# Optimization experiments

Hardware: AMD Instinct MI355X
Metric: run time of the kernel (lower is better)

Reference implementation:

```python
import jax, jax.numpy as jnp
import numpy as np
jax.config.update("jax_enable_x64", True)

B, S, E, H, L, FF = 2, 1024, 768, 12, 4, 2048
MAX_THOUGHT_LEN = 3
LN_EPS = 1e-5

def _sinusoidal_pe(max_len, d):
    pos = np.arange(max_len)[:, None]
    div = np.exp(np.arange(0, d, 2) * (-np.log(10000.0) / d))
    pe = np.zeros((max_len, d), np.float32)
    pe[:, 0::2] = np.sin(pos * div)
    pe[:, 1::2] = np.cos(pos * div)
    return jnp.asarray(pe)

def _build_mask(Smax, thoughts_taken, n_tokens):
    # Vectorized equivalent of the torch loop building the block-causal mask.
    bs = thoughts_taken + 1
    i = np.arange(Smax)[:, None]
    j = np.arange(Smax)[None, :]
    same_block = (i // bs == j // bs) & (i // bs < n_tokens) & ((i % bs) >= (j % bs))
    start_vis = ((j % bs) == 0) & (j // bs < n_tokens) & (i > j) & (i < n_tokens * bs)
    allowed = same_block | start_vis
    # TransformerEncoder canonicalizes the bool mask: True (disallowed) -> -inf additive
    return jnp.asarray(np.where(allowed, 0.0, -np.inf).astype(np.float64))

def _layernorm(x, w, b):
    mu = jnp.mean(x, -1, keepdims=True)
    var = jnp.mean((x - mu) ** 2, -1, keepdims=True)
    return (x - mu) / jnp.sqrt(var + LN_EPS) * w + b

def setup_inputs() -> dict:
    key = jax.random.key(0)
    ks = jax.random.split(key, 8)
    f32 = jnp.float32
    return {
        "x": jax.random.normal(ks[0], (B, S, E), f32),
        "padding_mask": jnp.zeros((B, S), bool),
        "thought_pe": jax.random.normal(ks[1], (MAX_THOUGHT_LEN + 1, E), f32),
        "Wqkv": jax.random.normal(ks[2], (L, 3 * E, E), f32) * (E ** -0.5),
        "bqkv": jnp.zeros((L, 3 * E), f32),
        "W1": jax.random.normal(ks[3], (L, FF, E), f32) * (E ** -0.5),
        "b1": jnp.zeros((L, FF), f32),
        "W2": jax.random.normal(ks[4], (L, E, FF), f32) * (FF ** -0.5),
        "b2": jnp.zeros((L, E), f32),
        "ln1_w": jnp.ones((L, E), f32), "ln1_b": jnp.zeros((L, E), f32),
        "ln2_w": jnp.ones((L, E), f32), "ln2_b": jnp.zeros((L, E), f32),
        "lnf_w": jnp.ones((E,), f32), "lnf_b": jnp.zeros((E,), f32),
        "thoughts_taken": 1,
        "real_token_count": 512,
    }

def reference(x, padding_mask, thought_pe, Wqkv, bqkv, W1, b1, W2, b2,
              ln1_w, ln1_b, ln2_w, ln2_b, lnf_w, lnf_b,
              thoughts_taken, real_token_count):
    # NOTE: padding_mask is accepted but unused, matching the custom layer.
    nt = thoughts_taken + 1
    pe = _sinusoidal_pe(S, E)
    # DualPositionalEncoding (eval mode -> dropout is identity)
    h = x[:, : real_token_count * nt].reshape(B, real_token_count, nt, E)
    h = h + pe[:real_token_count][None, :, None, :] + thought_pe[:nt][None, None, :, :]
    h = h.reshape(B, real_token_count * nt, E)
    pad = S - real_token_count * nt
    if pad > 0:
        h = jnp.pad(h, ((0, 0), (0, pad), (0, 0)))
    mask = _build_mask(S, thoughts_taken, real_token_count)
    scale = 1.0 / jnp.sqrt(jnp.float64(E // H))
    for l in range(L):
        # manual fp64 attention, exactly as the torch layer
        s64 = h.astype(jnp.float64)
        qkv = s64 @ Wqkv[l].astype(jnp.float64).T + bqkv[l].astype(jnp.float64)
        q, k, v = jnp.split(qkv, 3, axis=-1)
        rh = lambda t: t.reshape(B, S, H, E // H).transpose(0, 2, 1, 3)
        q, k, v = rh(q), rh(k), rh(v)
        scores = jnp.einsum("bhqd,bhkd->bhqk", q, k) * scale + mask
        attn = jax.nn.softmax(scores, axis=-1)
        ao = jnp.einsum("bhqk,bhkd->bhqd", attn, v).transpose(0, 2, 1, 3).reshape(B, S, E)
        # NOTE: no out_proj -- the custom forward skips self_attn.out_proj
        h = _layernorm(h + ao.astype(h.dtype), ln1_w[l], ln1_b[l])
        ff = jax.nn.gelu(h @ W1[l].T + b1[l], approximate=False) @ W2[l].T + b2[l]
        h = _layernorm(h + ff, ln2_w[l], ln2_b[l])
        h = jnp.nan_to_num(h)
    return _layernorm(h, lnf_w, lnf_b)
```

## Files before the change

kernel.cpp:

```cpp
#include <hip/hip_runtime.h>
#include <math.h>

#define SEQ 1024
#define EMB 768
#define NHEAD 12
#define HDIM 64
#define NLAYER 4
#define FFDIM 2048
#define BATCH 2
#define ROWS (BATCH * SEQ)
#define BH (BATCH * NHEAD)
#define NCHUNK 2
#define CTILES 8

using f16 = _Float16;
using f16x4 = __attribute__((ext_vector_type(4))) _Float16;
using f16x8 = __attribute__((ext_vector_type(8))) _Float16;
using f32x4 = __attribute__((ext_vector_type(4))) float;
using f32x16 = __attribute__((ext_vector_type(16))) float;
typedef unsigned long long u64;

__device__ inline void gload16(const void* g, void* l) {
    __builtin_amdgcn_global_load_lds((const __attribute__((address_space(1))) unsigned*)g,
                                     (__attribute__((address_space(3))) unsigned*)l, 16, 0, 0);
}

__global__ void prep_kernel(const float* __restrict__ Wq, int na,
                            const float* __restrict__ W1, int nb,
                            const float* __restrict__ W2, int nc,
                            f16* __restrict__ oq, f16* __restrict__ o1, f16* __restrict__ o2,
                            const float* __restrict__ x,
                            const float* __restrict__ tpe,
                            float* __restrict__ h32,
                            f16* __restrict__ h16,
                            u64* __restrict__ mtab,
                            const int* __restrict__ tt_p,
                            const int* __restrict__ rtc_p) {
    const int ncast = na + nb + nc;
    const int nembed = BATCH * SEQ * EMB;
    const int nmask = SEQ * 16;
    const int total = ncast + nembed + nmask;
    const int nt = *tt_p + 1;
    const int rtc = *rtc_p;
    for (int i = blockIdx.x * blockDim.x + threadIdx.x; i < total;
         i += gridDim.x * blockDim.x) {
        if (i < ncast) {
            const float* src;
            f16* dst;
            int off;
            if (i < na)            { src = Wq; dst = oq; off = i; }
            else if (i < na + nb)  { src = W1; dst = o1; off = i - na; }
            else                   { src = W2; dst = o2; off = i - na - nb; }
            float4 v = ((const float4*)src)[off];
            f16x4 o;
            o[0] = (f16)v.x; o[1] = (f16)v.y; o[2] = (f16)v.z; o[3] = (f16)v.w;
            ((f16x4*)dst)[off] = o;
        } else if (i < ncast + nembed) {
            int idx = i - ncast;
            int e = idx % EMB;
            int s = (idx / EMB) % SEQ;
            float val;
            if (s < rtc * nt) {
                int p = s / nt;
                int t = s % nt;
                int i2 = e & ~1;
                float div = __expf((float)i2 * -0.0119926314f);
                float ang = (float)p * div;
                float pe = (e & 1) ? __cosf(ang) : __sinf(ang);
                val = x[idx] + pe + tpe[t * EMB + e];
            } else {
                val = 0.0f;
            }
            h32[idx] = val;
            h16[idx] = (f16)val;
        } else {
            int idx = i - ncast - nembed;
            int ii = idx >> 4, jt = idx & 15;
            int id = ii / nt, im = ii % nt;
            int iok = (ii < rtc * nt);
            u64 m = 0;
            for (int k = 0; k < 64; k++) {
                int j = jt * 64 + k;
                int jd = j / nt, jm = j % nt;
                bool same = (id == jd) && (id < rtc) && (im >= jm);
                bool sv   = (jm == 0) && (jd < rtc) && (ii > j) && iok;
                if (same || sv) m |= (1ull << k);
            }
            mtab[idx] = m;
        }
    }
}

template<int ACT, int OUT>
__global__ __launch_bounds__(512) void gemm_f16(const f16* __restrict__ A,
                                                const f16* __restrict__ W,
                                                const float* __restrict__ bias,
                                                f16* __restrict__ Ch,
                                                f16* __restrict__ vtg,
                                                int M, int N, int K) {
    __shared__ f16 As[2][128 * 64];
    __shared__ f16 Ws[2][128 * 64];
    const int tid = threadIdx.x, lane = tid & 63, wave = tid >> 6;
    const int gx = gridDim.x;
    const int nwg = gx * gridDim.y;
    int orig = blockIdx.y * gx + blockIdx.x;
    int nid = (nwg & 7) ? orig : ((orig & 7) * (nwg >> 3) + (orig >> 3));
    const int bm = (nid / gx) * 128, bn = (nid % gx) * 128;
    const int l31 = lane & 31, l32 = lane >> 5;
    const int wm = (wave >> 1) * 32, wn = (wave & 1) * 64;
    const int srow = lane >> 3, sslot = lane & 7;
    const int klen = K / gridDim.z;
    const int kbeg = blockIdx.z * klen;
    const int nsteps = klen >> 6;

    f32x16 acc[2];
#pragma unroll
    for (int ni = 0; ni < 2; ni++)
#pragma unroll
        for (int e = 0; e < 16; e++) acc[ni][e] = 0.f;

#pragma unroll
    for (int i = 0; i < 2; i++) {
        int R0 = wave * 16 + i * 8;
        int row = R0 + srow;
        int gs = (sslot ^ (row & 7)) << 3;
        gload16(A + (size_t)(bm + row) * K + kbeg + gs, As[0] + R0 * 64);
        gload16(W + (size_t)(bn + row) * K + kbeg + gs, Ws[0] + R0 * 64);
    }
    __syncthreads();

    int cur = 0;
    for (int t = 0; t < nsteps; t++) {
        if (t + 1 < nsteps) {
            int k1 = kbeg + (t + 1) * 64;
            int nxt = cur ^ 1;
#pragma unroll
            for (int i = 0; i < 2; i++) {
                int R0 = wave * 16 + i * 8;
                int row = R0 + srow;
                int gs = (sslot ^ (row & 7)) << 3;
                gload16(A + (size_t)(bm + row) * K + k1 + gs, As[nxt] + R0 * 64);
                gload16(W + (size_t)(bn + row) * K + k1 + gs, Ws[nxt] + R0 * 64);
            }
        }
#pragma unroll
        for (int ks = 0; ks < 4; ks++) {
            int kslot = ks * 2 + l32;
            f16x8 a, b[2];
            {
                int row = wm + l31;
                a = *(const f16x8*)(As[cur] + row * 64 + ((kslot ^ (row & 7)) << 3));
            }
#pragma unroll
            for (int ni = 0; ni < 2; ni++) {
                int row = wn + ni * 32 + l31;
                b[ni] = *(const f16x8*)(Ws[cur] + row * 64 + ((kslot ^ (row & 7)) << 3));
            }
#pragma unroll
            for (int ni = 0; ni < 2; ni++)
                acc[ni] = __builtin_amdgcn_mfma_f32_32x32x16_f16(a, b[ni], acc[ni], 0, 0, 0);
        }
        __syncthreads();
        cur ^= 1;
    }

#pragma unroll
    for (int ni = 0; ni < 2; ni++) {
        int nbase = bn + wn + ni * 32;
        int n = nbase + l31;
        if (OUT == 3) {
            f16* dst = Ch + (size_t)blockIdx.z * ROWS * N;
#pragma unroll
            for (int reg = 0; reg < 16; reg++) {
                int m = bm + wm + (reg & 3) + 8 * (reg >> 2) + 4 * l32;
                dst[(size_t)m * N + n] = (f16)acc[ni][reg];
            }
        } else {
            float bv = bias[n];
            if (OUT != 2 || nbase < 2 * EMB) {
                int cstride = (OUT == 2) ? 2 * EMB : N;
#pragma unroll
                for (int reg = 0; reg < 16; reg++) {
                    int m = bm + wm + (reg & 3) + 8 * (reg >> 2) + 4 * l32;
                    float v = acc[ni][reg] + bv;
                    if (ACT) v = 0.5f * v * (1.0f + erff(v * 0.70710678118654752f));
                    Ch[(size_t)m * cstride + n] = (f16)v;
                }
            } else {
                int d = n - 2 * EMB;
                int hh = d >> 6, dd = d & 63;
#pragma unroll
                for (int q = 0; q < 4; q++) {
                    int m0 = bm + wm + 8 * q + 4 * l32;
                    int bb = m0 >> 10, s0 = m0 & (SEQ - 1);
                    f16x4 pack;
#pragma unroll
                    for (int r = 0; r < 4; r++) pack[r] = (f16)(acc[ni][4 * q + r] + bv);
                    *(f16x4*)(vtg + ((size_t)((bb * NHEAD + hh) * HDIM + dd)) * SEQ + s0) = pack;
                }
            }
        }
    }
}

__global__ __launch_bounds__(256) void attn_part(const f16* __restrict__ qk,
                                                 const f16* __restrict__ vtg,
                                                 const u64* __restrict__ mtab,
                                                 f16* __restrict__ po,
                                                 float* __restrict__ pm,
                                                 float* __restrict__ pl) {
    const int c = blockIdx.x;
    const int qt = blockIdx.y;
    if (c * CTILES > qt) return;
    const int bh = blockIdx.z;
    const int b = bh / NHEAD, hh = bh % NHEAD;
    const int q0 = qt * 64;
    const int jt_beg = c * CTILES, jt_end = min(qt, c * CTILES + CTILES - 1);

    __shared__ f16 Qs[64 * 64];
    __shared__ f16 Ks[2][64 * 64];
    __shared__ f16 VT[2][64 * 64];
    __shared__ f16 Ps[4 * 16 * 64];

    const int tid = threadIdx.x, lane = tid & 63, wave = tid >> 6;
    const int l15 = lane & 15, l16 = lane >> 4;
    const int RS = 2 * EMB;
    const f16* vth = vtg + (size_t)(b * NHEAD + hh) * HDIM * SEQ;
    const float SCALE2 = 0.125f * 1.44269504088896f;

#pragma unroll
    for (int it = 0; it < 2; it++) {
        int R0 = wave * 16 + it * 8;
        int row = R0 + (lane >> 3), slot = lane & 7;
        int gs = (slot ^ (row & 7)) << 3;
        gload16(qk + (size_t)(b * SEQ + q0 + row) * RS + hh * HDIM + gs, Qs + R0 * 64);
        gload16(qk + (size_t)(b * SEQ + jt_beg * 64 + row) * RS + EMB + hh * HDIM + gs,
                Ks[0] + R0 * 64);
        gload16(vth + (size_t)row * SEQ + jt_beg * 64 + gs, VT[0] + R0 * 64);
    }
    __syncthreads();

    f16x8 qa[2];
#pragma unroll
    for (int ks = 0; ks < 2; ks++) {
        int row = wave * 16 + l15;
        int kslot = l16 + ks * 4;
        qa[ks] = *(const f16x8*)(Qs + row * 64 + ((kslot ^ (row & 7)) << 3));
    }

    f16x8 ones;
#pragma unroll
    for (int i = 0; i < 8; i++) ones[i] = (f16)1.0f;

    float mrow[4];
    f32x4 o[4], osum;
    int iglob[4];
#pragma unroll
    for (int r = 0; r < 4; r++) {
        mrow[r] = -1e30f;
        iglob[r] = q0 + wave * 16 + l16 * 4 + r;
    }
#pragma unroll
    for (int nf = 0; nf < 4; nf++) o[nf] = (f32x4){0.f, 0.f, 0.f, 0.f};
    osum = (f32x4){0.f, 0.f, 0.f, 0.f};

    for (int jt = jt_beg; jt <= jt_end; jt++) {
        const int cur = (jt - jt_beg) & 1;
        if (jt < jt_end) {
            const int nxt = cur ^ 1;
            const int jn0 = (jt + 1) * 64;
#pragma unroll
            for (int it = 0; it < 2; it++) {
                int R0 = wave * 16 + it * 8;
                int row = R0 + (lane >> 3), slot = lane & 7;
                int gs = (slot ^ (row & 7)) << 3;
                gload16(qk + (size_t)(b * SEQ + jn0 + row) * RS + EMB + hh * HDIM + gs,
                        Ks[nxt] + R0 * 64);
                gload16(vth + (size_t)row * SEQ + jn0 + gs, VT[nxt] + R0 * 64);
            }
        }

        unsigned mlo[4], mhi[4];
#pragma unroll
        for (int r = 0; r < 4; r++) {
            u64 mk = mtab[iglob[r] * 16 + jt];
            mlo[r] = (unsigned)mk;
            mhi[r] = (unsigned)(mk >> 32);
        }

        f32x4 s[4];
        __builtin_amdgcn_s_setprio(1);
#pragma unroll
        for (int nf = 0; nf < 4; nf++) {
            s[nf] = (f32x4){0.f, 0.f, 0.f, 0.f};
#pragma unroll
            for (int ks = 0; ks < 2; ks++) {
                int row = nf * 16 + l15;
                int kslot = l16 + ks * 4;
                f16x8 kb = *(const f16x8*)(Ks[cur] + row * 64 + ((kslot ^ (row & 7)) << 3));
                s[nf] = __builtin_amdgcn_mfma_f32_16x16x32_f16(qa[ks], kb, s[nf], 0, 0, 0);
            }
        }
        __builtin_amdgcn_s_setprio(0);

        float p[4][4];
        float tmax[4] = {-1e30f, -1e30f, -1e30f, -1e30f};
#pragma unroll
        for (int nf = 0; nf < 4; nf++) {
            int sh = (nf & 1) * 16 + l15;
#pragma unroll
            for (int r = 0; r < 4; r++) {
                unsigned w = (nf & 2) ? mhi[r] : mlo[r];
                bool allowed = (w >> sh) & 1;
                float val = allowed ? s[nf][r] * SCALE2 : -1e30f;
                p[nf][r] = val;
                tmax[r] = fmaxf(tmax[r], val);
            }
        }
#pragma unroll
        for (int r = 0; r < 4; r++) {
            tmax[r] = fmaxf(tmax[r], __shfl_xor(tmax[r], 1));
            tmax[r] = fmaxf(tmax[r], __shfl_xor(tmax[r], 2));
            tmax[r] = fmaxf(tmax[r], __shfl_xor(tmax[r], 4));
            tmax[r] = fmaxf(tmax[r], __shfl_xor(tmax[r], 8));
        }
        float alpha[4], meff[4];
#pragma unroll
        for (int r = 0; r < 4; r++) {
            float mn = fmaxf(mrow[r], tmax[r]);
            alpha[r] = exp2f(mrow[r] - mn);
            mrow[r] = mn;
            meff[r] = (mn <= -1e29f) ? 0.f : mn;
        }
#pragma unroll
        for (int nf = 0; nf < 4; nf++)
#pragma unroll
            for (int r = 0; r < 4; r++)
                p[nf][r] = exp2f(p[nf][r] - meff[r]);
#pragma unroll
        for (int r = 0; r < 4; r++) osum[r] *= alpha[r];
#pragma unroll
        for (int nf = 0; nf < 4; nf++)
#pragma unroll
            for (int r = 0; r < 4; r++) o[nf][r] *= alpha[r];

        f16* P = Ps + wave * 16 * 64;
#pragma unroll
        for (int nf = 0; nf < 4; nf++)
#pragma unroll
            for (int r = 0; r < 4; r++) {
                int prow = l16 * 4 + r;
                int pcol = nf * 16 + l15;
                P[prow * 64 + (((pcol >> 3) ^ (prow & 7)) << 3) + (pcol & 7)] = (f16)p[nf][r];
            }

        __builtin_amdgcn_s_setprio(1);
#pragma unroll
        for (int ks = 0; ks < 2; ks++) {
            int kslot = l16 + ks * 4;
            int prow = l15;
            f16x8 pa = *(const f16x8*)(P + prow * 64 + ((kslot ^ (prow & 7)) << 3));
            osum = __builtin_amdgcn_mfma_f32_16x16x32_f16(pa, ones, osum, 0, 0, 0);
#pragma unroll
            for (int nf = 0; nf < 4; nf++) {
                int vrow = nf * 16 + l15;
                f16x8 vb = *(const f16x8*)(VT[cur] + vrow * 64 + ((kslot ^ (vrow & 7)) << 3));
                o[nf] = __builtin_amdgcn_mfma_f32_16x16x32_f16(pa, vb, o[nf], 0, 0, 0);
            }
        }
        __builtin_amdgcn_s_setprio(0);
        __syncthreads();
    }

    const size_t base = (size_t)(c * BH + bh) * SEQ;
#pragma unroll
    for (int r = 0; r < 4; r++) {
        int i = q0 + wave * 16 + l16 * 4 + r;
#pragma unroll
        for (int nf = 0; nf < 4; nf++)
            po[(base + i) * 64 + nf * 16 + l15] = (f16)o[nf][r];
        if (l15 == 0) {
            pm[base + i] = mrow[r];
            pl[base + i] = osum[r];
        }
    }
}

__global__ __launch_bounds__(256) void add_ln_attn(const float* __restrict__ X,
                                                   const f16* __restrict__ po,
                                                   const float* __restrict__ pm,
                                                   const float* __restrict__ pl,
                                                   const float* __restrict__ w,
                                                   const float* __restrict__ bsh,
                                                   float* __restrict__ out32,
                                                   f16* __restrict__ out16) {
    const int row = blockIdx.x * 4 + (threadIdx.x >> 6);
    const int lane = threadIdx.x & 63;
    const int b = row >> 10, i = row & (SEQ - 1);
    const int nch = (i >> 6) / CTILES + 1;
    const float* xr = X + (size_t)row * EMB;
    float4 v[3];
    float s = 0.f;
#pragma unroll
    for (int t = 0; t < 3; t++) {
        int e = t * 256 + lane * 4;
        int hh = e >> 6, d = e & 63;
        size_t hbase = (size_t)(b * NHEAD + hh) * SEQ + i;
        float m = -1e30f;
        for (int c = 0; c < nch; c++) m = fmaxf(m, pm[hbase + (size_t)c * BH * SEQ]);
        float meff = (m <= -1e29f) ? 0.f : m;
        float lt = 0.f;
        float4 ov = {0.f, 0.f, 0.f, 0.f};
        for (int c = 0; c < nch; c++) {
            size_t idx = hbase + (size_t)c * BH * SEQ;
            float wgt = exp2f(pm[idx] - meff);
            lt += pl[idx] * wgt;
            f16x4 pv = *(const f16x4*)(po + idx * 64 + d);
            ov.x += (float)pv[0] * wgt; ov.y += (float)pv[1] * wgt;
            ov.z += (float)pv[2] * wgt; ov.w += (float)pv[3] * wgt;
        }
        float inv = (lt > 0.f) ? 1.0f / lt : 0.0f;
        float4 a = *(const float4*)(xr + e);
        a.x += ov.x * inv; a.y += ov.y * inv; a.z += ov.z * inv; a.w += ov.w * inv;
        v[t] = a;
        s += a.x + a.y + a.z + a.w;
    }
#pragma unroll
    for (int k = 1; k < 64; k <<= 1) s += __shfl_xor(s, k);
    float mu = s * (1.0f / EMB);
    float s2 = 0.f;
#pragma unroll
    for (int t = 0; t < 3; t++) {
        float dx = v[t].x - mu, dy = v[t].y - mu, dz = v[t].z - mu, dw = v[t].w - mu;
        s2 += dx * dx + dy * dy + dz * dz + dw * dw;
    }
#pragma unroll
    for (int k = 1; k < 64; k <<= 1) s2 += __shfl_xor(s2, k);
    float inv = rsqrtf(s2 * (1.0f / EMB) + 1e-5f);
#pragma unroll
    for (int t = 0; t < 3; t++) {
        int e = t * 256 + lane * 4;
        float4 wv = *(const float4*)(w + e);
        float4 bv = *(const float4*)(bsh + e);
        float4 o;
        o.x = (v[t].x - mu) * inv * wv.x + bv.x;
        o.y = (v[t].y - mu) * inv * wv.y + bv.y;
        o.z = (v[t].z - mu) * inv * wv.z + bv.z;
        o.w = (v[t].w - mu) * inv * wv.w + bv.w;
        *(float4*)(out32 + (size_t)row * EMB + e) = o;
        f16x4 hh;
        hh[0] = (f16)o.x; hh[1] = (f16)o.y; hh[2] = (f16)o.z; hh[3] = (f16)o.w;
        *(f16x4*)(out16 + (size_t)row * EMB + e) = hh;
    }
}

template<int FINAL>
__global__ __launch_bounds__(256) void add_ln_split4(const float* __restrict__ X,
                                                     const f16* __restrict__ part,
                                                     const float* __restrict__ bias,
                                                     const float* __restrict__ w,
                                                     const float* __restrict__ bsh,
                                                     const float* __restrict__ wf,
                                                     const float* __restrict__ bf,
                                                     float* __restrict__ out32,
                                                     f16* __restrict__ out16) {
    const int row = blockIdx.x * 4 + (threadIdx.x >> 6);
    const int lane = threadIdx.x & 63;
    const float* xr = X + (size_t)row * EMB;
    float4 v[3];
    float s = 0.f;
#pragma unroll
    for (int t = 0; t < 3; t++) {
        int e = t * 256 + lane * 4;
        float4 a = *(const float4*)(xr + e);
        float4 bb = *(const float4*)(bias + e);
        a.x += bb.x; a.y += bb.y; a.z += bb.z; a.w += bb.w;
#pragma unroll
        for (int z = 0; z < 4; z++) {
            f16x4 pz = *(const f16x4*)(part + (size_t)z * ROWS * EMB + (size_t)row * EMB + e);
            a.x += (float)pz[0]; a.y += (float)pz[1];
            a.z += (float)pz[2]; a.w += (float)pz[3];
        }
        v[t] = a;
        s += a.x + a.y + a.z + a.w;
    }
#pragma unroll
    for (int k = 1; k < 64; k <<= 1) s += __shfl_xor(s, k);
    float mu = s * (1.0f / EMB);
    float s2 = 0.f;
#pragma unroll
    for (int t = 0; t < 3; t++) {
        float dx = v[t].x - mu, dy = v[t].y - mu, dz = v[t].z - mu, dw = v[t].w - mu;
        s2 += dx * dx + dy * dy + dz * dz + dw * dw;
    }
#pragma unroll
    for (int k = 1; k < 64; k <<= 1) s2 += __shfl_xor(s2, k);
    float inv = rsqrtf(s2 * (1.0f / EMB) + 1e-5f);
    float4 o2[3];
    float sF = 0.f;
#pragma unroll
    for (int t = 0; t < 3; t++) {
        int e = t * 256 + lane * 4;
        float4 wv = *(const float4*)(w + e);
        float4 bv = *(const float4*)(bsh + e);
        float4 o;
        o.x = (v[t].x - mu) * inv * wv.x + bv.x;
        o.y = (v[t].y - mu) * inv * wv.y + bv.y;
        o.z = (v[t].z - mu) * inv * wv.z + bv.z;
        o.w = (v[t].w - mu) * inv * wv.w + bv.w;
        o2[t] = o;
        if (FINAL) sF += o.x + o.y + o.z + o.w;
        else {
            *(float4*)(out32 + (size_t)row * EMB + e) = o;
            f16x4 hh;
            hh[0] = (f16)o.x; hh[1] = (f16)o.y; hh[2] = (f16)o.z; hh[3] = (f16)o.w;
            *(f16x4*)(out16 + (size_t)row * EMB + e) = hh;
        }
    }
    if (FINAL) {
#pragma unroll
        for (int k = 1; k < 64; k <<= 1) sF += __shfl_xor(sF, k);
        float muF = sF * (1.0f / EMB);
        float s2F = 0.f;
#pragma unroll
        for (int t = 0; t < 3; t++) {
            float dx = o2[t].x - muF, dy = o2[t].y - muF, dz = o2[t].z - muF, dw = o2[t].w - muF;
            s2F += dx * dx + dy * dy + dz * dz + dw * dw;
        }
#pragma unroll
        for (int k = 1; k < 64; k <<= 1) s2F += __shfl_xor(s2F, k);
        float invF = rsqrtf(s2F * (1.0f / EMB) + 1e-5f);
#pragma unroll
        for (int t = 0; t < 3; t++) {
            int e = t * 256 + lane * 4;
            float4 wv = *(const float4*)(wf + e);
            float4 bv = *(const float4*)(bf + e);
            float4 o;
            o.x = (o2[t].x - muF) * invF * wv.x + bv.x;
            o.y = (o2[t].y - muF) * invF * wv.y + bv.y;
            o.z = (o2[t].z - muF) * invF * wv.z + bv.z;
            o.w = (o2[t].w - muF) * invF * wv.w + bv.w;
            *(float4*)(out32 + (size_t)row * EMB + e) = o;
        }
    }
}

extern "C" void kernel_launch(void* const* d_in, const int* in_sizes, int n_in,
                              void* d_out, int out_size, void* d_ws, size_t ws_size,
                              hipStream_t stream) {
    const float* x      = (const float*)d_in[0];
    const float* tpe    = (const float*)d_in[2];
    const float* Wqkv   = (const float*)d_in[3];
    const float* bqkv   = (const float*)d_in[4];
    const float* W1     = (const float*)d_in[5];
    const float* b1     = (const float*)d_in[6];
    const float* W2     = (const float*)d_in[7];
    const float* b2     = (const float*)d_in[8];
    const float* ln1_w  = (const float*)d_in[9];
    const float* ln1_b  = (const float*)d_in[10];
    const float* ln2_w  = (const float*)d_in[11];
    const float* ln2_b  = (const float*)d_in[12];
    const float* lnf_w  = (const float*)d_in[13];
    const float* lnf_b  = (const float*)d_in[14];
    const int*   tt     = (const int*)d_in[15];
    const int*   rtc    = (const int*)d_in[16];
    float* out = (float*)d_out;

    char* wsp = (char*)d_ws;
    float* h32  = (float*)wsp;
    f16*   h16  = (f16*)(wsp + 6291456);
    f16*   act  = (f16*)(wsp + 9437184);
    f16*   vtg  = (f16*)(wsp + 17825792);
    f16*   part = (f16*)(wsp + 20971520);
    f16*   wbuf = (f16*)(wsp + 33554432);
    f16*   po   = (f16*)(wsp + 72876032);
    float* pm   = (float*)(wsp + 79167488);
    float* pl   = (float*)(wsp + 79364096);
    u64*   mtab = (u64*)(wsp + 79560704);

    const int EQ = 3 * EMB * EMB;
    const int E1 = FFDIM * EMB;
    const int E2 = EMB * FFDIM;
    f16* wqAll = wbuf;
    f16* w1All = wbuf + (size_t)NLAYER * EQ;
    f16* w2All = w1All + (size_t)NLAYER * E1;

    prep_kernel<<<4096, 256, 0, stream>>>(Wqkv, NLAYER * EQ / 4, W1, NLAYER * E1 / 4,
                                          W2, NLAYER * E2 / 4, wqAll, w1All, w2All,
                                          x, tpe, h32, h16, mtab, tt, rtc);

    for (int l = 0; l < NLAYER; l++) {
        const f16* wq16 = wqAll + (size_t)l * EQ;
        const f16* w116 = w1All + (size_t)l * E1;
        const f16* w216 = w2All + (size_t)l * E2;
        const float* bq  = bqkv + (size_t)l * 3 * EMB;
        const float* bb1 = b1 + (size_t)l * FFDIM;
        const float* bb2 = b2 + (size_t)l * EMB;

        gemm_f16<0, 2><<<dim3(3 * EMB / 128, ROWS / 128), 512, 0, stream>>>(
            h16, wq16, bq, act, vtg, ROWS, 3 * EMB, EMB);

        attn_part<<<dim3(NCHUNK, SEQ / 64, BH), 256, 0, stream>>>(act, vtg, mtab, po, pm, pl);

        add_ln_attn<<<ROWS / 4, 256, 0, stream>>>(h32, po, pm, pl,
                                                  ln1_w + l * EMB, ln1_b + l * EMB, h32, h16);

        gemm_f16<1, 1><<<dim3(FFDIM / 128, ROWS / 128), 512, 0, stream>>>(
            h16, w116, bb1, act, nullptr, ROWS, FFDIM, EMB);

        gemm_f16<0, 3><<<dim3(EMB / 128, ROWS / 128, 4), 512, 0, stream>>>(
            act, w216, nullptr, part, nullptr, ROWS, EMB, FFDIM);

        if (l < NLAYER - 1)
            add_ln_split4<0><<<ROWS / 4, 256, 0, stream>>>(h32, part, bb2,
                ln2_w + l * EMB, ln2_b + l * EMB, nullptr, nullptr, h32, h16);
        else
            add_ln_split4<1><<<ROWS / 4, 256, 0, stream>>>(h32, part, bb2,
                ln2_w + l * EMB, ln2_b + l * EMB, lnf_w, lnf_b, out, nullptr);
    }
}
```

Measured before the change: 386.7 us.

## Read Q/K/V fragments directly from global memory in attention kernel

Removes the LDS staging and double-buffered async prefetch of Q, K and V^T tiles in attn_part. Each wave now loads its MFMA operand fragments straight from global memory and relies on cache reuse across the four waves, which also drops the per-iteration block barrier. This frees shared memory, which may raise occupancy, but it multiplies global/L2 traffic, since every wave reloads the whole K/V tile, and it loses the overlap of loads with compute.

```diff
diff --git a/kernel.cpp b/kernel.cpp
--- a/kernel.cpp
+++ b/kernel.cpp
@@ -217,35 +217,20 @@
     const int q0 = qt * 64;
     const int jt_beg = c * CTILES, jt_end = min(qt, c * CTILES + CTILES - 1);
 
-    __shared__ f16 Qs[64 * 64];
-    __shared__ f16 Ks[2][64 * 64];
-    __shared__ f16 VT[2][64 * 64];
     __shared__ f16 Ps[4 * 16 * 64];
 
     const int tid = threadIdx.x, lane = tid & 63, wave = tid >> 6;
     const int l15 = lane & 15, l16 = lane >> 4;
     const int RS = 2 * EMB;
     const f16* vth = vtg + (size_t)(b * NHEAD + hh) * HDIM * SEQ;
+    const f16* kh  = qk + EMB + hh * HDIM;
     const float SCALE2 = 0.125f * 1.44269504088896f;
 
-#pragma unroll
-    for (int it = 0; it < 2; it++) {
-        int R0 = wave * 16 + it * 8;
-        int row = R0 + (lane >> 3), slot = lane & 7;
-        int gs = (slot ^ (row & 7)) << 3;
-        gload16(qk + (size_t)(b * SEQ + q0 + row) * RS + hh * HDIM + gs, Qs + R0 * 64);
-        gload16(qk + (size_t)(b * SEQ + jt_beg * 64 + row) * RS + EMB + hh * HDIM + gs,
-                Ks[0] + R0 * 64);
-        gload16(vth + (size_t)row * SEQ + jt_beg * 64 + gs, VT[0] + R0 * 64);
-    }
-    __syncthreads();
-
     f16x8 qa[2];
 #pragma unroll
     for (int ks = 0; ks < 2; ks++) {
-        int row = wave * 16 + l15;
-        int kslot = l16 + ks * 4;
-        qa[ks] = *(const f16x8*)(Qs + row * 64 + ((kslot ^ (row & 7)) << 3));
+        int row = q0 + wave * 16 + l15;
+        qa[ks] = *(const f16x8*)(qk + (size_t)(b * SEQ + row) * RS + hh * HDIM + (l16 + ks * 4) * 8);
     }
 
     f16x8 ones;
@@ -265,20 +250,7 @@
     osum = (f32x4){0.f, 0.f, 0.f, 0.f};
 
     for (int jt = jt_beg; jt <= jt_end; jt++) {
-        const int cur = (jt - jt_beg) & 1;
-        if (jt < jt_end) {
-            const int nxt = cur ^ 1;
-            const int jn0 = (jt + 1) * 64;
-#pragma unroll
-            for (int it = 0; it < 2; it++) {
-                int R0 = wave * 16 + it * 8;
-                int row = R0 + (lane >> 3), slot = lane & 7;
-                int gs = (slot ^ (row & 7)) << 3;
-                gload16(qk + (size_t)(b * SEQ + jn0 + row) * RS + EMB + hh * HDIM + gs,
-                        Ks[nxt] + R0 * 64);
-                gload16(vth + (size_t)row * SEQ + jn0 + gs, VT[nxt] + R0 * 64);
-            }
-        }
+        const int j0 = jt * 64;
 
         unsigned mlo[4], mhi[4];
 #pragma unroll
@@ -295,9 +267,8 @@
             s[nf] = (f32x4){0.f, 0.f, 0.f, 0.f};
 #pragma unroll
             for (int ks = 0; ks < 2; ks++) {
-                int row = nf * 16 + l15;
-                int kslot = l16 + ks * 4;
-                f16x8 kb = *(const f16x8*)(Ks[cur] + row * 64 + ((kslot ^ (row & 7)) << 3));
+                f16x8 kb = *(const f16x8*)(kh + (size_t)(b * SEQ + j0 + nf * 16 + l15) * RS
+                                              + (l16 + ks * 4) * 8);
                 s[nf] = __builtin_amdgcn_mfma_f32_16x16x32_f16(qa[ks], kb, s[nf], 0, 0, 0);
             }
         }
@@ -363,13 +334,11 @@
             osum = __builtin_amdgcn_mfma_f32_16x16x32_f16(pa, ones, osum, 0, 0, 0);
 #pragma unroll
             for (int nf = 0; nf < 4; nf++) {
-                int vrow = nf * 16 + l15;
-                f16x8 vb = *(const f16x8*)(VT[cur] + vrow * 64 + ((kslot ^ (vrow & 7)) << 3));
+                f16x8 vb = *(const f16x8*)(vth + (size_t)(nf * 16 + l15) * SEQ + j0 + kslot * 8);
                 o[nf] = __builtin_amdgcn_mfma_f32_16x16x32_f16(pa, vb, o[nf], 0, 0, 0);
             }
         }
         __builtin_amdgcn_s_setprio(0);
-        __syncthreads();
     }
 
     const size_t base = (size_t)(c * BH + bh) * SEQ;
```

After: 484.0 us. +25.2%, slower.
